# Optimization experiments

Measured on AMD Instinct MI355X. Metric: run time of the kernel, lower is better.

The kernel has to match this reference:

```python
import jax, jax.numpy as jnp
import numpy as np

B, S, D = 8, 1024, 512


def setup_inputs() -> dict:
    key = jax.random.key(0)
    k1, k2, k3, k4, k5, k6, k7 = jax.random.split(key, 7)
    inp = jax.random.normal(k1, (B, S, D), dtype=jnp.float32)
    aspect = jax.random.normal(k2, (B, S, D), dtype=jnp.float32)
    # lengths in [S//2, S], with max exactly S (the module requires max(len)==S)
    inp_len = jax.random.randint(k3, (B,), S // 2, S + 1).astype(jnp.float32)
    inp_len = inp_len.at[0].set(float(S))
    lim = float(np.sqrt(6.0 / (D + D)))  # xavier_uniform bound
    w1 = jax.random.uniform(k4, (D, D), jnp.float32, -lim, lim)
    b1 = jax.random.uniform(k5, (D,), jnp.float32, -lim, lim)
    w2 = jax.random.uniform(k6, (D, D), jnp.float32, -lim, lim)
    b2 = jax.random.uniform(k7, (D,), jnp.float32, -lim, lim)
    return {"inp": inp, "inp_len": inp_len, "aspect": aspect,
            "w1": w1, "b1": b1, "w2": w2, "b2": b2}


def reference(inp, inp_len, aspect, w1, b1, w2, b2):
    # inp, aspect: [B,S,D]; inp_len: [B] float lengths with max == S
    Bv, Sv, Dv = inp.shape
    scale = jnp.sqrt(inp_len)[:, None, None]                      # [B,1,1]
    att = jnp.einsum('bsd,btd->bst', aspect, inp) / scale          # [B,S,S]
    # mask over the query (row) dimension, as in the original expand
    mask = (jnp.arange(Sv)[None, :] < inp_len.astype(jnp.int32)[:, None]).astype(inp.dtype)  # [B,S]
    exp = att * mask[:, :, None]
    att_n = exp / (jnp.sum(exp, axis=-1, keepdims=True) + 1e-4)    # linear (non-exp) normalize
    weighted = jnp.einsum('bst,btd->bsd', att_n, inp)              # [B,S,D]
    ffn_inp = weighted + (inp + aspect) * mask[:, :, None]
    # FFN: two square linears with relu, plus inner residual
    o1 = jax.nn.relu(jnp.einsum('bsd,ed->bse', ffn_inp, w1) + b1)
    o2 = jax.nn.relu(jnp.einsum('bsd,ed->bse', o1, w2) + b2)
    ffn_out = o2 + ffn_inp
    final = ffn_inp + ffn_out
    return final / jnp.linalg.norm(final, axis=2, keepdims=True)
```

## Files before the change

kernel.cpp:

```cpp
#include <hip/hip_runtime.h>

#define Bq 8
#define Sq 1024
#define Dq 512

typedef __attribute__((ext_vector_type(8))) short bf16x8;
typedef __attribute__((ext_vector_type(4))) float f32x4;

__device__ __forceinline__ unsigned short f2bf(float f) {
  unsigned int u = __float_as_uint(f);
  return (unsigned short)((u + 0x7fffu + ((u >> 16) & 1u)) >> 16);
}

__device__ __forceinline__ void load_lds16(const unsigned short* g, unsigned short* l) {
  __builtin_amdgcn_global_load_lds(
      (const __attribute__((address_space(1))) unsigned int*)g,
      (__attribute__((address_space(3))) unsigned int*)l, 16, 0, 0);
}


__global__ __launch_bounds__(256) void prep_t(
    const float* __restrict__ inp,
    unsigned short* __restrict__ inpT, float* __restrict__ partial) {
  __shared__ unsigned short tile[64][66];
  __shared__ float csum[16][64];
  int idx = blockIdx.x;
  int tid = threadIdx.x;
  int b = idx & 7, tt = (idx >> 3) & 15, dd = idx >> 7;
  int r = tid >> 4, c4 = (tid & 15) * 4;
  const float* src = inp + ((size_t)b * Sq + tt * 64) * Dq + dd * 64;
  float cp0 = 0.f, cp1 = 0.f, cp2 = 0.f, cp3 = 0.f;
#pragma unroll
  for (int p = 0; p < 4; ++p) {
    float4 v = *(const float4*)(src + (size_t)(r + p * 16) * Dq + c4);
    ushort4 o; o.x = f2bf(v.x); o.y = f2bf(v.y); o.z = f2bf(v.z); o.w = f2bf(v.w);
    *(ushort4*)&tile[r + p * 16][c4] = o;
    cp0 += v.x; cp1 += v.y; cp2 += v.z; cp3 += v.w;
  }
  csum[r][c4] = cp0; csum[r][c4 + 1] = cp1; csum[r][c4 + 2] = cp2; csum[r][c4 + 3] = cp3;
  __syncthreads();
  unsigned short* dst = inpT + (size_t)b * Dq * Sq + (size_t)dd * 64 * Sq + tt * 64;
#pragma unroll
  for (int p = 0; p < 4; ++p) {
    int d = (tid >> 4) + p * 16;
    int tq = (tid & 15) * 4;
    ushort4 o;
    o.x = tile[tq][d]; o.y = tile[tq + 1][d]; o.z = tile[tq + 2][d]; o.w = tile[tq + 3][d];
    *(ushort4*)(dst + (size_t)d * Sq + tq) = o;
  }
  if (tid < 64) {
    float s = 0.f;
#pragma unroll
    for (int rr = 0; rr < 16; ++rr) s += csum[rr][tid];
    partial[((size_t)b * 16 + tt) * Dq + dd * 64 + tid] = s;
  }
}

__global__ __launch_bounds__(512, 2) void gram_fac(
    const unsigned short* __restrict__ inpT, const float* __restrict__ partial,
    const float* __restrict__ aspect, const float* __restrict__ lenv,
    const float* __restrict__ w1, const float* __restrict__ w2,
    unsigned short* __restrict__ Gm, float* __restrict__ fac,
    unsigned short* __restrict__ asp_bf,
    unsigned short* __restrict__ w1b, unsigned short* __restrict__ w2b) {
  __shared__ unsigned short sA[2][64 * 64];
  __shared__ unsigned short sB[2][128 * 64];
  int idx = blockIdx.x;
  int tid = threadIdx.x;
  int lane = tid & 63, wave = tid >> 6;

  if (idx >= 768) {
    int blk = idx - 768;
    const float* src = (blk < 128) ? w1 : w2;
    unsigned short* dst = (blk < 128) ? w1b : w2b;
    int li = ((blk & 127) * 512 + tid) * 4;
    int n = li >> 9, k = li & 511;
    float4 v = *(const float4*)(src + li);
    ushort4 o; o.x = f2bf(v.x); o.y = f2bf(v.y); o.z = f2bf(v.z); o.w = f2bf(v.w);
    int x = ((k >> 3) & 3) ^ ((n >> 1) & 3);
    int off = (k >> 5) * 16384 + n * 32 + x * 8 + (k & 7);
    *(ushort4*)(dst + off) = o;
    return;
  }
  if (idx >= 512) {
    int blk = idx - 512;
    const float* s = aspect + (size_t)blk * 16384 + tid * 4;
    unsigned short* d = asp_bf + (size_t)blk * 16384 + tid * 4;
#pragma unroll
    for (int j = 0; j < 8; ++j) {
      float4 v = *(const float4*)(s + j * 2048);
      ushort4 o; o.x = f2bf(v.x); o.y = f2bf(v.y); o.z = f2bf(v.z); o.w = f2bf(v.w);
      *(ushort4*)(d + j * 2048) = o;
    }
    return;
  }
  if (idx >= 256) {
    float* cs = (float*)sA;
    int fblk = idx - 256;
    int b = fblk >> 5;
    int s0 = (fblk & 31) * 32;
    {
      int d = tid;
      float s = 0.f;
      const float* p = partial + (size_t)b * 16 * Dq + d;
#pragma unroll
      for (int t = 0; t < 16; ++t) s += p[t * Dq];
      cs[d] = s;
    }
    __syncthreads();
    int g = lane >> 4, lr = lane & 15;
    int row = s0 + wave * 4 + g;
    const float* a = aspect + ((size_t)b * Sq + row) * Dq + lr * 32;
    float sum = 0.f;
#pragma unroll
    for (int j = 0; j < 8; ++j) {
      float4 v = *(const float4*)(a + j * 4);
      const float* c = cs + lr * 32 + j * 4;
      sum += v.x * c[0] + v.y * c[1] + v.z * c[2] + v.w * c[3];
    }
#pragma unroll
    for (int off = 1; off < 16; off <<= 1) sum += __shfl_xor(sum, off, 64);
    if (lr == 0) {
      float len = lenv[b];
      float scale = sqrtf(len);
      float f = 0.f;
      if (row < (int)len) f = 1.f / (scale * (sum / scale + 1e-4f));
      fac[b * Sq + row] = f;
    }
    return;
  }

  const int K = 1024;
  int b = idx & 7;
  int tile = idx >> 3;
  int bm = tile & 7, bn = tile >> 3;
  const unsigned short* Ab = inpT + (size_t)b * Dq * Sq + (size_t)bm * 64 * K;
  const unsigned short* Bb = inpT + (size_t)b * Dq * Sq + (size_t)bn * 128 * K;
  int lr = lane & 15, lq = lane >> 4;
  int x7 = lr & 7;
  int t8 = tid >> 3, t7 = tid & 7;

  const unsigned short* gA = Ab + (size_t)t8 * K + (t7 ^ (t8 & 7)) * 8;
  const unsigned short* gB = Bb + (size_t)t8 * K + (t7 ^ (t8 & 7)) * 8;
  const unsigned short* gB2 = Bb + (size_t)(t8 + 64) * K + (t7 ^ (t8 & 7)) * 8;
  int dbase = tid * 8;

  f32x4 acc[2][2] = {};

  auto issue = [&](int buf, int k0) {
    load_lds16(gA + k0, &sA[buf][dbase]);
    load_lds16(gB + k0, &sB[buf][dbase]);
    load_lds16(gB2 + k0, &sB[buf][4096 + dbase]);
  };

  int wm = (wave & 1) * 32, wn = (wave >> 1) * 32;
  issue(0, 0);
#pragma unroll
  for (int it = 0; it < 16; ++it) {
    int cur = it & 1;
    if (it + 1 < 16) {
      issue(cur ^ 1, (it + 1) << 6);
      asm volatile("s_waitcnt vmcnt(3)" ::: "memory");
    } else {
      asm volatile("s_waitcnt vmcnt(0)" ::: "memory");
    }
    __builtin_amdgcn_s_barrier();
#pragma unroll
    for (int c = 0; c < 2; ++c) {
      int g = (c * 4 + lq) ^ x7;
      bf16x8 a0 = *(const bf16x8*)&sA[cur][((wm + lr) * 8 + g) * 8];
      bf16x8 a1 = *(const bf16x8*)&sA[cur][((wm + 16 + lr) * 8 + g) * 8];
      bf16x8 b0 = *(const bf16x8*)&sB[cur][((wn + lr) * 8 + g) * 8];
      bf16x8 b1 = *(const bf16x8*)&sB[cur][((wn + 16 + lr) * 8 + g) * 8];
      acc[0][0] = __builtin_amdgcn_mfma_f32_16x16x32_bf16(a0, b0, acc[0][0], 0, 0, 0);
      acc[0][1] = __builtin_amdgcn_mfma_f32_16x16x32_bf16(a0, b1, acc[0][1], 0, 0, 0);
      acc[1][0] = __builtin_amdgcn_mfma_f32_16x16x32_bf16(a1, b0, acc[1][0], 0, 0, 0);
      acc[1][1] = __builtin_amdgcn_mfma_f32_16x16x32_bf16(a1, b1, acc[1][1], 0, 0, 0);
    }
    asm volatile("s_waitcnt lgkmcnt(0)" ::: "memory");
    __builtin_amdgcn_sched_barrier(0);
    __builtin_amdgcn_s_barrier();
  }

  unsigned short* sP = sB[0];
  int kcl = wm >> 5;
#pragma unroll
  for (int mi = 0; mi < 2; ++mi)
#pragma unroll
    for (int ni = 0; ni < 2; ++ni)
#pragma unroll
      for (int i = 0; i < 4; ++i) {
        int rl = mi * 16 + lq * 4 + i;
        int nl = wn + ni * 16 + lr;
        int x = (rl >> 3) ^ ((nl >> 1) & 3);
        sP[kcl * 4096 + nl * 32 + x * 8 + (rl & 7)] = f2bf(acc[mi][ni][i]);
      }
  __syncthreads();
  unsigned short* Ob = Gm + (size_t)b * 512 * 512 + (size_t)(bm * 2) * 16384 +
                       (size_t)bn * 4096;
#pragma unroll
  for (int h = 0; h < 2; ++h)
    *(bf16x8*)(Ob + h * 16384 + tid * 8) = *(const bf16x8*)(sP + h * 4096 + tid * 8);
}

__global__ __launch_bounds__(512, 2) void mega_ffn(
    const unsigned short* __restrict__ aspb, const unsigned short* __restrict__ G,
    const unsigned short* __restrict__ w1b, const unsigned short* __restrict__ w2b,
    const float* __restrict__ b1, const float* __restrict__ b2,
    const float* __restrict__ inp, const float* __restrict__ aspect,
    const float* __restrict__ fac, const float* __restrict__ lenv,
    float* __restrict__ out) {
  __shared__ unsigned short ldsA[32 * 512];
  __shared__ float ssqW[8 * 32];
  int tid = threadIdx.x;
  int lane = tid & 63, wave = tid >> 6;
  int lr = lane & 15, lq = lane >> 4;
  int batch = blockIdx.x & 7;
  int pos = blockIdx.x >> 3;
  int r0 = batch * 1024 + pos * 32;
  int c0 = wave * 64;

  f32x4 acc[2][4];
  float ffnv[2][4][4];

  auto aoff = [&](int rr, int c) {
    int cq = c >> 3;
    return rr * 512 + ((cq ^ (rr & 7)) << 3) + (c & 7);
  };
  auto baddr = [&](const unsigned short* Bp, int kc, int cc) {
    return Bp + kc * 16384 + cc * 32 + ((lq ^ ((cc >> 1) & 3)) << 3);
  };

  auto gemmPhase = [&](const unsigned short* Bp) {
    bf16x8 bq[3][4];
    bf16x8 aq[2][2];
#pragma unroll
    for (int m = 0; m < 2; ++m)
#pragma unroll
      for (int t = 0; t < 4; ++t) acc[m][t] = (f32x4){0.f, 0.f, 0.f, 0.f};
#pragma unroll
    for (int t = 0; t < 4; ++t) {
      bq[0][t] = *(const bf16x8*)baddr(Bp, 0, c0 + t * 16 + lr);
      bq[1][t] = *(const bf16x8*)baddr(Bp, 1, c0 + t * 16 + lr);
    }
#pragma unroll
    for (int m = 0; m < 2; ++m)
      aq[0][m] = *(const bf16x8*)&ldsA[aoff(m * 16 + lr, lq * 8)];
#pragma unroll
    for (int kc = 0; kc < 16; ++kc) {
      if (kc + 2 < 16) {
#pragma unroll
        for (int t = 0; t < 4; ++t)
          bq[(kc + 2) % 3][t] = *(const bf16x8*)baddr(Bp, kc + 2, c0 + t * 16 + lr);
      }
      if (kc + 1 < 16) {
#pragma unroll
        for (int m = 0; m < 2; ++m)
          aq[(kc + 1) & 1][m] =
              *(const bf16x8*)&ldsA[aoff(m * 16 + lr, (kc + 1) * 32 + lq * 8)];
      }
      __builtin_amdgcn_s_setprio(1);
#pragma unroll
      for (int t = 0; t < 4; ++t) {
        acc[0][t] = __builtin_amdgcn_mfma_f32_16x16x32_bf16(aq[kc & 1][0], bq[kc % 3][t],
                                                            acc[0][t], 0, 0, 0);
        acc[1][t] = __builtin_amdgcn_mfma_f32_16x16x32_bf16(aq[kc & 1][1], bq[kc % 3][t],
                                                            acc[1][t], 0, 0, 0);
      }
      __builtin_amdgcn_s_setprio(0);
    }
  };

#pragma unroll
  for (int h = 0; h < 8; ++h) {
    int s = h * 512 + tid;
    int rr = s >> 6, sq = s & 63;
    int cq = sq ^ (rr & 7);
    load_lds16(aspb + (size_t)(r0 + rr) * 512 + cq * 8, ldsA + s * 8);
  }
  asm volatile("s_waitcnt vmcnt(0)" ::: "memory");
  __syncthreads();

  gemmPhase(G + (size_t)batch * 512 * 512);
  int len = (int)lenv[batch];
  float facv[2][4];
#pragma unroll
  for (int m = 0; m < 2; ++m)
#pragma unroll
    for (int i = 0; i < 4; ++i) facv[m][i] = fac[r0 + m * 16 + lq * 4 + i];
  __syncthreads();
#pragma unroll
  for (int m = 0; m < 2; ++m)
#pragma unroll
    for (int t = 0; t < 4; ++t)
#pragma unroll
      for (int i = 0; i < 4; ++i) {
        int rr = m * 16 + lq * 4 + i;
        int gr = r0 + rr;
        size_t idx = (size_t)gr * 512 + c0 + t * 16 + lr;
        float add = ((gr & 1023) < len) ? (inp[idx] + aspect[idx]) : 0.f;
        float v = acc[m][t][i] * facv[m][i] + add;
        ffnv[m][t][i] = v;
        ldsA[aoff(rr, c0 + t * 16 + lr)] = f2bf(v);
      }
  __syncthreads();

  gemmPhase(w1b);
  float biasv[4];
#pragma unroll
  for (int t = 0; t < 4; ++t) biasv[t] = b1[c0 + t * 16 + lr];
  __syncthreads();
#pragma unroll
  for (int m = 0; m < 2; ++m)
#pragma unroll
    for (int t = 0; t < 4; ++t)
#pragma unroll
      for (int i = 0; i < 4; ++i) {
        int rr = m * 16 + lq * 4 + i;
        ldsA[aoff(rr, c0 + t * 16 + lr)] = f2bf(fmaxf(acc[m][t][i] + biasv[t], 0.f));
      }
  __syncthreads();

  gemmPhase(w2b);
#pragma unroll
  for (int t = 0; t < 4; ++t) biasv[t] = b2[c0 + t * 16 + lr];
  float ssq[2][4] = {{0.f, 0.f, 0.f, 0.f}, {0.f, 0.f, 0.f, 0.f}};
#pragma unroll
  for (int m = 0; m < 2; ++m)
#pragma unroll
    for (int t = 0; t < 4; ++t)
#pragma unroll
      for (int i = 0; i < 4; ++i) {
        float v = 2.f * ffnv[m][t][i] + fmaxf(acc[m][t][i] + biasv[t], 0.f);
        ffnv[m][t][i] = v;
        ssq[m][i] += v * v;
      }
#pragma unroll
  for (int off = 1; off < 16; off <<= 1)
#pragma unroll
    for (int m = 0; m < 2; ++m)
#pragma unroll
      for (int i = 0; i < 4; ++i) ssq[m][i] += __shfl_xor(ssq[m][i], off, 64);
  if (lr == 0)
#pragma unroll
    for (int m = 0; m < 2; ++m)
#pragma unroll
      for (int i = 0; i < 4; ++i) ssqW[wave * 32 + m * 16 + lq * 4 + i] = ssq[m][i];
  __syncthreads();
  float rn[2][4];
#pragma unroll
  for (int m = 0; m < 2; ++m)
#pragma unroll
    for (int i = 0; i < 4; ++i) {
      float s = 0.f;
#pragma unroll
      for (int w = 0; w < 8; ++w) s += ssqW[w * 32 + m * 16 + lq * 4 + i];
      rn[m][i] = 1.f / sqrtf(s);
    }
#pragma unroll
  for (int m = 0; m < 2; ++m)
#pragma unroll
    for (int t = 0; t < 4; ++t)
#pragma unroll
      for (int i = 0; i < 4; ++i) {
        int gr = r0 + m * 16 + lq * 4 + i;
        out[(size_t)gr * 512 + c0 + t * 16 + lr] = ffnv[m][t][i] * rn[m][i];
      }
}

extern "C" void kernel_launch(void* const* d_in, const int* in_sizes, int n_in,
                              void* d_out, int out_size, void* d_ws, size_t ws_size,
                              hipStream_t stream) {
  const float* inp = (const float*)d_in[0];
  const float* inp_len = (const float*)d_in[1];
  const float* aspect = (const float*)d_in[2];
  const float* w1 = (const float*)d_in[3];
  const float* b1 = (const float*)d_in[4];
  const float* w2 = (const float*)d_in[5];
  const float* b2 = (const float*)d_in[6];
  float* out = (float*)d_out;

  char* W = (char*)d_ws;
  const size_t MB = 1ull << 20;
  unsigned short* asp_bf = (unsigned short*)(W + 0);
  unsigned short* inpT   = (unsigned short*)(W + 8 * MB);
  unsigned short* Gm     = (unsigned short*)(W + 16 * MB);
  unsigned short* w1bf   = (unsigned short*)(W + 20 * MB);
  unsigned short* w2bf   = (unsigned short*)(W + 20 * MB + 512 * 1024);
  float*          partial= (float*)(W + 21 * MB);
  float*          fac    = (float*)(W + 22 * MB);

  prep_t<<<1024, 256, 0, stream>>>(inp, inpT, partial);

  gram_fac<<<1024, 512, 0, stream>>>(inpT, partial, aspect, inp_len, w1, w2,
                                     Gm, fac, asp_bf, w1bf, w2bf);

  mega_ffn<<<256, 512, 0, stream>>>(
      asp_bf, Gm, w1bf, w2bf, b1, b2, inp, aspect, fac, inp_len, out);
}
```

Baseline: 132.1 us.

## Stream FFN weight tiles through triple-buffered LDS via direct global-to-LDS loads

In the fused FFN kernel, B-operand (weight/Gram) fragments were loaded from global memory straight into registers with a 3-deep register prefetch. They now go through a per-wave triple-buffered LDS region filled by global_load_lds, with explicit vmcnt waits, and are read back from LDS before each MFMA step. The A fragments are also read per iteration instead of being double-buffered in registers. The aim is to cut VGPR pressure and hide global latency through asynchronous copies. The cost is about 130KB of dynamic shared memory, occupancy dropping to one block per CU, and a hipFuncSetAttribute call on every launch.

After: 132.9 us. Within noise of the previous version (+0.6%).

```diff
diff --git a/kernel.cpp b/kernel.cpp
--- a/kernel.cpp
+++ b/kernel.cpp
@@ -203,15 +203,19 @@
     *(bf16x8*)(Ob + h * 16384 + tid * 8) = *(const bf16x8*)(sP + h * 4096 + tid * 8);
 }
 
-__global__ __launch_bounds__(512, 2) void mega_ffn(
+#define MEGA_SMEM (32768 + 3 * 32768 + 1024)
+
+__global__ __launch_bounds__(512, 1) void mega_ffn(
     const unsigned short* __restrict__ aspb, const unsigned short* __restrict__ G,
     const unsigned short* __restrict__ w1b, const unsigned short* __restrict__ w2b,
     const float* __restrict__ b1, const float* __restrict__ b2,
     const float* __restrict__ inp, const float* __restrict__ aspect,
     const float* __restrict__ fac, const float* __restrict__ lenv,
     float* __restrict__ out) {
-  __shared__ unsigned short ldsA[32 * 512];
-  __shared__ float ssqW[8 * 32];
+  extern __shared__ char smem[];
+  unsigned short* ldsA = (unsigned short*)smem;
+  unsigned short* wbuf = (unsigned short*)(smem + 32768);
+  float* ssqW = (float*)(smem + 32768 + 3 * 65536 / 2);
   int tid = threadIdx.x;
   int lane = tid & 63, wave = tid >> 6;
   int lr = lane & 15, lq = lane >> 4;
@@ -227,45 +231,45 @@
     int cq = c >> 3;
     return rr * 512 + ((cq ^ (rr & 7)) << 3) + (c & 7);
   };
-  auto baddr = [&](const unsigned short* Bp, int kc, int cc) {
-    return Bp + kc * 16384 + cc * 32 + ((lq ^ ((cc >> 1) & 3)) << 3);
+  int bx = (lq ^ ((lr >> 1) & 3)) * 8;
+  int rdbase = (c0 + lr) * 32 + bx;
+
+  auto stage = [&](int buf, int kc, const unsigned short* Bp) {
+    const unsigned short* src = Bp + kc * 16384 + wave * 2048 + lane * 8;
+    unsigned short* dst = wbuf + buf * 16384 + wave * 2048 + lane * 8;
+#pragma unroll
+    for (int i = 0; i < 4; ++i) load_lds16(src + i * 512, dst + i * 512);
   };
 
   auto gemmPhase = [&](const unsigned short* Bp) {
-    bf16x8 bq[3][4];
-    bf16x8 aq[2][2];
 #pragma unroll
     for (int m = 0; m < 2; ++m)
 #pragma unroll
       for (int t = 0; t < 4; ++t) acc[m][t] = (f32x4){0.f, 0.f, 0.f, 0.f};
-#pragma unroll
-    for (int t = 0; t < 4; ++t) {
-      bq[0][t] = *(const bf16x8*)baddr(Bp, 0, c0 + t * 16 + lr);
-      bq[1][t] = *(const bf16x8*)baddr(Bp, 1, c0 + t * 16 + lr);
-    }
-#pragma unroll
-    for (int m = 0; m < 2; ++m)
-      aq[0][m] = *(const bf16x8*)&ldsA[aoff(m * 16 + lr, lq * 8)];
+    stage(0, 0, Bp);
+    stage(1, 1, Bp);
 #pragma unroll
     for (int kc = 0; kc < 16; ++kc) {
-      if (kc + 2 < 16) {
-#pragma unroll
-        for (int t = 0; t < 4; ++t)
-          bq[(kc + 2) % 3][t] = *(const bf16x8*)baddr(Bp, kc + 2, c0 + t * 16 + lr);
-      }
-      if (kc + 1 < 16) {
-#pragma unroll
-        for (int m = 0; m < 2; ++m)
-          aq[(kc + 1) & 1][m] =
-              *(const bf16x8*)&ldsA[aoff(m * 16 + lr, (kc + 1) * 32 + lq * 8)];
-      }
+      int cur = kc % 3;
+      if (kc + 2 < 16) stage((kc + 2) % 3, kc + 2, Bp);
+      if (kc < 14) {
+        asm volatile("s_waitcnt vmcnt(8)" ::: "memory");
+      } else if (kc == 14) {
+        asm volatile("s_waitcnt vmcnt(4)" ::: "memory");
+      } else {
+        asm volatile("s_waitcnt vmcnt(0)" ::: "memory");
+      }
+      bf16x8 a0 = *(const bf16x8*)&ldsA[aoff(lr, kc * 32 + lq * 8)];
+      bf16x8 a1 = *(const bf16x8*)&ldsA[aoff(16 + lr, kc * 32 + lq * 8)];
+      bf16x8 bfr[4];
+#pragma unroll
+      for (int t = 0; t < 4; ++t)
+        bfr[t] = *(const bf16x8*)&wbuf[cur * 16384 + rdbase + t * 512];
       __builtin_amdgcn_s_setprio(1);
 #pragma unroll
       for (int t = 0; t < 4; ++t) {
-        acc[0][t] = __builtin_amdgcn_mfma_f32_16x16x32_bf16(aq[kc & 1][0], bq[kc % 3][t],
-                                                            acc[0][t], 0, 0, 0);
-        acc[1][t] = __builtin_amdgcn_mfma_f32_16x16x32_bf16(aq[kc & 1][1], bq[kc % 3][t],
-                                                            acc[1][t], 0, 0, 0);
+        acc[0][t] = __builtin_amdgcn_mfma_f32_16x16x32_bf16(a0, bfr[t], acc[0][t], 0, 0, 0);
+        acc[1][t] = __builtin_amdgcn_mfma_f32_16x16x32_bf16(a1, bfr[t], acc[1][t], 0, 0, 0);
       }
       __builtin_amdgcn_s_setprio(0);
     }
@@ -395,6 +399,8 @@
   gram_fac<<<1024, 512, 0, stream>>>(inpT, partial, aspect, inp_len, w1, w2,
                                      Gm, fac, asp_bf, w1bf, w2bf);
 
-  mega_ffn<<<256, 512, 0, stream>>>(
+  hipFuncSetAttribute((const void*)mega_ffn,
+                      hipFuncAttributeMaxDynamicSharedMemorySize, MEGA_SMEM);
+  mega_ffn<<<256, 512, MEGA_SMEM, stream>>>(
       asp_bf, Gm, w1bf, w2bf, b1, b2, inp, aspect, fac, inp_len, out);
 }
```
